# Performance work log

Measured on AMD Instinct MI355X. Metric: run time of the kernel, lower is better.

## Reference

```python
import jax, jax.numpy as jnp
import numpy as np

N, M, D, G, E = 1024, 1024, 1024, 16, 64  # rois, ref rois, feat_dim, groups, emb_dim
DG = D // G  # 64 per-group dim


def _make_boxes(k, n):
    k1, k2 = jax.random.split(k)
    xy = jax.random.uniform(k1, (n, 2), dtype=jnp.float32) * 500.0
    wh = jax.random.uniform(k2, (n, 2), dtype=jnp.float32) * 100.0 + 1.0
    return jnp.concatenate([xy, xy + wh], axis=1)  # [n,4] xmin,ymin,xmax,ymax


def setup_inputs() -> dict:
    key = jax.random.key(0)
    ks = jax.random.split(key, 10)
    s = 0.02
    return {
        "roi_feat": jax.random.normal(ks[0], (N, D), dtype=jnp.float32),
        "ref_feat": jax.random.normal(ks[1], (M, D), dtype=jnp.float32),
        "rois1": _make_boxes(ks[2], N),
        "rois2": _make_boxes(ks[3], M),
        "Wq": jax.random.normal(ks[4], (D, D), dtype=jnp.float32) * s,
        "bq": jnp.zeros((D,), jnp.float32),
        "Wk": jax.random.normal(ks[5], (D, D), dtype=jnp.float32) * s,
        "bk": jnp.zeros((D,), jnp.float32),
        "Wg": jax.random.normal(ks[6], (G, E), dtype=jnp.float32) * s,
        "bg": jnp.zeros((G,), jnp.float32),
        "Wv": jax.random.normal(ks[7], (G, DG, D), dtype=jnp.float32) * s,
        "bv": jnp.zeros((D,), jnp.float32),
    }


def _position_matrix(bbox, ref_bbox):
    # bbox [N,4], ref_bbox [M,4] -> [N,M,4]
    def parts(b):
        xmin, ymin, xmax, ymax = b[:, 0], b[:, 1], b[:, 2], b[:, 3]
        w = xmax - xmin + 1.0
        h = ymax - ymin + 1.0
        cx = 0.5 * (xmin + xmax)
        cy = 0.5 * (ymin + ymax)
        return w, h, cx, cy

    w, h, cx, cy = parts(bbox)            # [N]
    wr, hr, cxr, cyr = parts(ref_bbox)    # [M]
    dx = jnp.log(jnp.abs((cx[:, None] - cxr[None, :]) / w[:, None]) + 1e-3)
    dy = jnp.log(jnp.abs((cy[:, None] - cyr[None, :]) / h[:, None]) + 1e-3)
    dw = jnp.log(w[:, None] / wr[None, :])
    dh = jnp.log(h[:, None] / hr[None, :])
    return jnp.stack([dx, dy, dw, dh], axis=2)  # [N,M,4]


def _position_embedding(pos_mat, feat_dim=64, wave_length=1000.0):
    fr = jnp.arange(feat_dim // 8, dtype=jnp.float32)            # [8]
    dim_mat = jnp.power(wave_length, (8.0 / feat_dim) * fr)      # [8]
    div = pos_mat[..., None] * 100.0 / dim_mat                   # [N,M,4,8]
    emb = jnp.concatenate([jnp.sin(div), jnp.cos(div)], axis=3)  # [N,M,4,16]
    return emb.reshape(pos_mat.shape[0], pos_mat.shape[1], -1)   # [N,M,64]


def reference(roi_feat, ref_feat, rois1, rois2, Wq, bq, Wk, bk, Wg, bg, Wv, bv):
    # position embedding: [N,M,E]
    pos_emb = _position_embedding(_position_matrix(rois1, rois2), feat_dim=E)
    # Wgs 1x1 conv (E -> G) + relu -> aff_weight [N,G,M]
    aff_weight = jax.nn.relu(jnp.einsum("nme,ge->ngm", pos_emb, Wg) + bg[None, :, None])
    # grouped q/k projections
    q = (roi_feat @ Wq + bq).reshape(N, G, DG)   # [N,G,dg]
    k = (ref_feat @ Wk + bk).reshape(M, G, DG)   # [M,G,dg]
    aff = jnp.einsum("ngd,mgd->ngm", q, k) * (1.0 / np.sqrt(DG))
    weighted = jnp.log(aff_weight + 1e-6) + aff  # [N,G,M]
    sm = jax.nn.softmax(weighted, axis=2)
    out_t = jnp.einsum("ngm,md->ngd", sm, ref_feat)          # [N,G,D]
    out = jnp.einsum("ngd,god->ngo", out_t, Wv).reshape(N, D) + bv  # grouped 1x1 conv
    return out
```

## Files before the change

### kernel.cpp

```cpp
#include <hip/hip_runtime.h>
#include <hip/hip_fp16.h>
#include <cstddef>

#define N_ 1024
#define M_ 1024
#define D_ 1024
#define G_ 16
#define DG_ 64

typedef __bf16 bf16x8 __attribute__((ext_vector_type(8)));
typedef _Float16 f16x8 __attribute__((ext_vector_type(8)));
typedef float f32x4 __attribute__((ext_vector_type(4)));

__device__ __forceinline__ size_t qkf_idx(int g, int rb, int ks, int lane) {
    return ((((size_t)(g * 64 + rb)) * 2 + ks) * 64 + lane) * 8;
}
__device__ __forceinline__ size_t vf_idx(int g, int ot, int mc, int lane) {
    return ((((size_t)(g * 4 + ot)) * 32 + mc) * 64 + lane) * 8;
}
__device__ __forceinline__ size_t awt_idx(int g, int mb, int n, int quad) {
    return (((size_t)(mb * 1024 + n)) * 16 + g) * 16 + quad * 4;
}

__global__ __launch_bounds__(256)
void fused_mid2(const float* __restrict__ roi, const float* __restrict__ ref,
                const float* __restrict__ Wq, const float* __restrict__ Wk,
                const float* __restrict__ Wv,
                const float* __restrict__ bq, const float* __restrict__ bk,
                __bf16* __restrict__ Qf, __bf16* __restrict__ Kf,
                __bf16* __restrict__ Vf,
                const float* __restrict__ rois1, const float* __restrict__ rois2,
                const float* __restrict__ Wg, const float* __restrict__ bg,
                __half* __restrict__ AWt)
{
    __shared__ __align__(16) char smem[36864];
    const int b = blockIdx.x;
    const int tid = threadIdx.x;
    const int w = tid >> 6, lane = tid & 63;
    const int quad = lane >> 4, l15 = lane & 15;

    if (b < 192) {
        const int t = b;
        const int z = t >> 6, t6 = t & 63;
        const float* A = (z == 0) ? roi : ref;
        const float* Wf = (z == 0) ? Wq : (z == 1) ? Wk : Wv;
        const int i0 = (t6 >> 3) * 128, j0 = (t6 & 7) * 128;
        const int iw = (w & 1) * 64, jw = (w >> 1) * 64;

        __bf16(*As)[72] = (__bf16(*)[72])smem;
        __bf16(*Bs)[72] = (__bf16(*)[72])(smem + 18432);

        f32x4 acc[4][4] = {};

        for (int k0 = 0; k0 < D_; k0 += 64) {
            __syncthreads();
            #pragma unroll
            for (int it = 0; it < 8; ++it) {
                const int idx = tid + 256 * it;
                const int row = idx >> 4, c = idx & 15;
                float4 a = *(const float4*)&A[(size_t)(i0 + row) * D_ + k0 + c * 4];
                __bf16 p[4] = {(__bf16)a.x, (__bf16)a.y, (__bf16)a.z, (__bf16)a.w};
                *(uint2*)&As[row][c * 4] = *(const uint2*)p;
            }
            if (z < 2) {
                #pragma unroll
                for (int it = 0; it < 8; ++it) {
                    const int idx = tid + 256 * it;
                    const int jl = idx & 127;
                    const int kc = idx >> 7;
                    const float* src = &Wf[(size_t)(k0 + kc * 4) * D_ + j0 + jl];
                    __bf16 p[4];
                    p[0] = (__bf16)src[0];
                    p[1] = (__bf16)src[D_];
                    p[2] = (__bf16)src[2 * D_];
                    p[3] = (__bf16)src[3 * D_];
                    *(uint2*)&Bs[jl][kc * 4] = *(const uint2*)p;
                }
            } else {
                #pragma unroll
                for (int it = 0; it < 8; ++it) {
                    const int idx = tid + 256 * it;
                    const int row = idx >> 4, c = idx & 15;
                    float4 a = *(const float4*)&Wf[(size_t)(j0 + row) * D_ + k0 + c * 4];
                    __bf16 p[4] = {(__bf16)a.x, (__bf16)a.y, (__bf16)a.z, (__bf16)a.w};
                    *(uint2*)&Bs[row][c * 4] = *(const uint2*)p;
                }
            }
            __syncthreads();
            #pragma unroll
            for (int ks = 0; ks < 2; ++ks) {
                bf16x8 af[4], bfr[4];
                #pragma unroll
                for (int t4 = 0; t4 < 4; ++t4) {
                    af[t4]  = *(const bf16x8*)&As[iw + t4 * 16 + l15][ks * 32 + quad * 8];
                    bfr[t4] = *(const bf16x8*)&Bs[jw + t4 * 16 + l15][ks * 32 + quad * 8];
                }
                #pragma unroll
                for (int ti = 0; ti < 4; ++ti)
                    #pragma unroll
                    for (int tj = 0; tj < 4; ++tj)
                        acc[ti][tj] = __builtin_amdgcn_mfma_f32_16x16x32_bf16(
                            af[ti], bfr[tj], acc[ti][tj], 0, 0, 0);
            }
        }

        if (z < 2) {
            const float* bias = (z == 0) ? bq : bk;
            __bf16* dst = (z == 0) ? Qf : Kf;
            const float scale = (z == 0) ? 0.125f : 1.0f;
            #pragma unroll
            for (int ti = 0; ti < 4; ++ti) {
                const int rb = (i0 + iw + ti * 16) >> 4;
                #pragma unroll
                for (int tj = 0; tj < 4; ++tj) {
                    const int go = j0 + jw + tj * 16 + l15;
                    const int g = go >> 6, ks = (go >> 5) & 1;
                    const int lanef = ((go >> 3) & 3) * 16;
                    const int jf = go & 7;
                    const float bb = bias[go];
                    __bf16* base = dst + qkf_idx(g, rb, ks, 0) + jf;
                    #pragma unroll
                    for (int r = 0; r < 4; ++r)
                        base[(size_t)(lanef + quad * 4 + r) * 8] =
                            (__bf16)((acc[ti][tj][r] + bb) * scale);
                }
            }
        } else {
            #pragma unroll
            for (int ti = 0; ti < 4; ++ti) {
                const int mbase = i0 + iw + ti * 16 + quad * 4;
                const int mc = mbase >> 5, quadv = (mbase >> 3) & 3, jb = mbase & 7;
                #pragma unroll
                for (int tj = 0; tj < 4; ++tj) {
                    const int go = j0 + jw + tj * 16 + l15;
                    const int g = go >> 6, ot = (go >> 4) & 3, o15 = go & 15;
                    __bf16 p[4];
                    #pragma unroll
                    for (int r = 0; r < 4; ++r) p[r] = (__bf16)acc[ti][tj][r];
                    *(uint2*)&Vf[vf_idx(g, ot, mc, quadv * 16 + o15) + jb] =
                        *(const uint2*)p;
                }
            }
        }
        return;
    }

    const int n = b - 192;

    const float xmin = rois1[n * 4 + 0], ymin = rois1[n * 4 + 1];
    const float xmax = rois1[n * 4 + 2], ymax = rois1[n * 4 + 3];
    const float wn  = xmax - xmin + 1.f, hn  = ymax - ymin + 1.f;
    const float cxn = 0.5f * (xmin + xmax), cyn = 0.5f * (ymin + ymax);
    const float rwn = 1.0f / wn, rhn = 1.0f / hn;
    const float lwn = __logf(wn), lhn = __logf(hn);

    f16x8 wgf[2];
    #pragma unroll
    for (int ks = 0; ks < 2; ++ks) {
        const float* p = &Wg[l15 * 64 + ks * 32 + quad * 8];
        float4 a = *(const float4*)p;
        float4 bb = *(const float4*)(p + 4);
        wgf[ks][0] = (_Float16)a.x; wgf[ks][1] = (_Float16)a.y;
        wgf[ks][2] = (_Float16)a.z; wgf[ks][3] = (_Float16)a.w;
        wgf[ks][4] = (_Float16)bb.x; wgf[ks][5] = (_Float16)bb.y;
        wgf[ks][6] = (_Float16)bb.z; wgf[ks][7] = (_Float16)bb.w;
    }
    const float bgv = bg[l15];

    const float fr8[8] = {100.0f, 42.16965f, 17.782794f, 7.4989421f,
                          3.1622777f, 1.3335214f, 0.56234133f, 0.23713737f};
    const float phase = (quad & 1) ? 1.5707963267948966f : 0.f;

    for (int mq = 0; mq < 4; ++mq) {
        const int m0w = mq * 256 + w * 64;
        #pragma unroll
        for (int ti = 0; ti < 4; ++ti) {
            const int mt0 = m0w + ti * 16;
            const int m = mt0 + l15;
            float4 r2 = *(const float4*)&rois2[m * 4];
            const float wr  = r2.z - r2.x + 1.f, hr  = r2.w - r2.y + 1.f;
            const float cxr = 0.5f * (r2.x + r2.z), cyr = 0.5f * (r2.y + r2.w);

            const float f0 = __logf(fabsf((cxn - cxr) * rwn) + 0.001f);
            const float f1 = __logf(fabsf((cyn - cyr) * rhn) + 0.001f);
            const float f2 = lwn - __logf(wr);
            const float f3 = lhn - __logf(hr);
            const float fa = (quad & 2) ? f1 : f0;
            const float fb = (quad & 2) ? f3 : f2;

            f32x4 acc = {};
            #pragma unroll
            for (int ks = 0; ks < 2; ++ks) {
                const float feat = ks ? fb : fa;
                f16x8 ef;
                #pragma unroll
                for (int j = 0; j < 8; ++j)
                    ef[j] = (_Float16)__sinf(fmaf(feat, fr8[j], phase));
                acc = __builtin_amdgcn_mfma_f32_16x16x32_f16(ef, wgf[ks], acc, 0, 0, 0);
            }

            __half p[4];
            #pragma unroll
            for (int r = 0; r < 4; ++r)
                p[r] = __float2half(fmaxf(acc[r] + bgv, 0.f) + 1e-6f);
            *(uint2*)&AWt[awt_idx(l15, mt0 >> 4, n, quad)] = *(const uint2*)p;
        }
    }
}

__global__ __launch_bounds__(256)
void attn_mfma(const __bf16* __restrict__ Qf, const __bf16* __restrict__ Kf,
               const __bf16* __restrict__ Vf, const __half* __restrict__ AWt,
               const float* __restrict__ bv, float* __restrict__ out)
{
    __shared__ __align__(16) char smem[17664];

    const int tid = threadIdx.x;
    const int w = tid >> 6, lane = tid & 63;
    const int quad = lane >> 4, l15 = lane & 15;
    const int nb = blockIdx.x, n0 = nb * 16, g = blockIdx.y;

    __bf16(*Psw)[72] = (__bf16(*)[72])(smem + w * 2304);
    float(*accb)[64][17] = (float(*)[64][17])smem;
    float(*lsb)[16] = (float(*)[16])(smem + 17408);

    bf16x8 qf[2];
    qf[0] = *(const bf16x8*)&Qf[qkf_idx(g, nb, 0, lane)];
    qf[1] = *(const bf16x8*)&Qf[qkf_idx(g, nb, 1, lane)];

    f32x4 acc[4] = {};
    float llocal = 0.f;

    #pragma unroll
    for (int t64 = 0; t64 < 4; ++t64) {
        const int mt = w * 4 + t64;

        f32x4 s[4];
        #pragma unroll
        for (int t = 0; t < 4; ++t) {
            bf16x8 ka0 = *(const bf16x8*)&Kf[qkf_idx(g, mt * 4 + t, 0, lane)];
            bf16x8 ka1 = *(const bf16x8*)&Kf[qkf_idx(g, mt * 4 + t, 1, lane)];
            f32x4 z = {};
            __builtin_amdgcn_s_setprio(1);
            z = __builtin_amdgcn_mfma_f32_16x16x32_bf16(ka0, qf[0], z, 0, 0, 0);
            s[t] = __builtin_amdgcn_mfma_f32_16x16x32_bf16(ka1, qf[1], z, 0, 0, 0);
            __builtin_amdgcn_s_setprio(0);
        }

        #pragma unroll
        for (int t = 0; t < 4; ++t) {
            uint2 au = *(const uint2*)&AWt[awt_idx(g, mt * 4 + t, n0 + l15, quad)];
            const __half* a4 = (const __half*)&au;
            __bf16 pk[4];
            #pragma unroll
            for (int r = 0; r < 4; ++r) {
                const float p = __half2float(a4[r]) * __expf(s[t][r]);
                llocal += p;
                pk[r] = (__bf16)p;
            }
            *(uint2*)&Psw[l15][t * 16 + quad * 4] = *(const uint2*)pk;
        }

        #pragma unroll
        for (int mcl = 0; mcl < 2; ++mcl) {
            bf16x8 pbf = *(const bf16x8*)&Psw[l15][mcl * 32 + quad * 8];
            __builtin_amdgcn_s_setprio(1);
            #pragma unroll
            for (int ot = 0; ot < 4; ++ot) {
                bf16x8 va = *(const bf16x8*)&Vf[vf_idx(g, ot, mt * 2 + mcl, lane)];
                acc[ot] = __builtin_amdgcn_mfma_f32_16x16x32_bf16(va, pbf, acc[ot], 0, 0, 0);
            }
            __builtin_amdgcn_s_setprio(0);
        }
    }

    llocal += __shfl_xor(llocal, 16, 64);
    llocal += __shfl_xor(llocal, 32, 64);

    __syncthreads();

    #pragma unroll
    for (int ot = 0; ot < 4; ++ot)
        #pragma unroll
        for (int r = 0; r < 4; ++r)
            accb[w][ot * 16 + quad * 4 + r][l15] = acc[ot][r];
    if (quad == 0) lsb[w][l15] = llocal;
    __syncthreads();

    const float lt = lsb[0][l15] + lsb[1][l15] + lsb[2][l15] + lsb[3][l15];
    const float inv = 1.f / lt;
    #pragma unroll
    for (int r = 0; r < 4; ++r) {
        const int o = w * 16 + quad * 4 + r;
        const int ogl = g * 64 + o;
        const float v = accb[0][o][l15] + accb[1][o][l15] +
                        accb[2][o][l15] + accb[3][o][l15];
        out[(size_t)(n0 + l15) * D_ + ogl] = v * inv + bv[ogl];
    }
}

extern "C" void kernel_launch(void* const* d_in, const int* in_sizes, int n_in,
                              void* d_out, int out_size, void* d_ws, size_t ws_size,
                              hipStream_t stream) {
    const float* roi_feat = (const float*)d_in[0];
    const float* ref_feat = (const float*)d_in[1];
    const float* rois1    = (const float*)d_in[2];
    const float* rois2    = (const float*)d_in[3];
    const float* Wq       = (const float*)d_in[4];
    const float* bq       = (const float*)d_in[5];
    const float* Wk       = (const float*)d_in[6];
    const float* bk       = (const float*)d_in[7];
    const float* Wg       = (const float*)d_in[8];
    const float* bg       = (const float*)d_in[9];
    const float* Wv       = (const float*)d_in[10];
    const float* bv       = (const float*)d_in[11];
    float* out = (float*)d_out;

    char* ws = (char*)d_ws;
    __bf16* Qf  = (__bf16*)(ws + 0);
    __bf16* Kf  = (__bf16*)(ws + (2u << 20));
    __bf16* Vf  = (__bf16*)(ws + (4u << 20));
    __half* AWt = (__half*)(ws + (6u << 20));

    dim3 blk(256);
    fused_mid2<<<dim3(1216), blk, 0, stream>>>(roi_feat, ref_feat, Wq, Wk, Wv,
                                               bq, bk, Qf, Kf, Vf,
                                               rois1, rois2, Wg, bg, AWt);
    attn_mfma<<<dim3(64, 16), blk, 0, stream>>>(Qf, Kf, Vf, AWt, bv, out);
}
```

Before: 137.7 us.

## Halve GEMM tile width and prefetch next K-slice into registers

The projection GEMM section now uses 128x64 output tiles instead of 128x128, doubling its block count from 192 to 384 so more CUs get work. It also adds register prefetching: the global loads for the next K-slice are issued right after the shared-memory stores, so they overlap the MFMA work on the current slice. Shared memory use drops to match the smaller B tile. In exchange, A tiles are re-read twice as often and register pressure rises from the prefetch buffers.

```diff
diff --git a/kernel.cpp b/kernel.cpp
--- a/kernel.cpp
+++ b/kernel.cpp
@@ -23,7 +23,7 @@
 }
 
 __global__ __launch_bounds__(256)
-void fused_mid2(const float* __restrict__ roi, const float* __restrict__ ref,
+void fused_mid3(const float* __restrict__ roi, const float* __restrict__ ref,
                 const float* __restrict__ Wq, const float* __restrict__ Wk,
                 const float* __restrict__ Wv,
                 const float* __restrict__ bq, const float* __restrict__ bk,
@@ -33,72 +33,129 @@
                 const float* __restrict__ Wg, const float* __restrict__ bg,
                 __half* __restrict__ AWt)
 {
-    __shared__ __align__(16) char smem[36864];
+    __shared__ __align__(16) char smem[27648];
     const int b = blockIdx.x;
     const int tid = threadIdx.x;
     const int w = tid >> 6, lane = tid & 63;
     const int quad = lane >> 4, l15 = lane & 15;
 
-    if (b < 192) {
-        const int t = b;
-        const int z = t >> 6, t6 = t & 63;
+    if (b < 384) {
+        const int z = b >> 7, t6 = b & 127;
         const float* A = (z == 0) ? roi : ref;
         const float* Wf = (z == 0) ? Wq : (z == 1) ? Wk : Wv;
-        const int i0 = (t6 >> 3) * 128, j0 = (t6 & 7) * 128;
-        const int iw = (w & 1) * 64, jw = (w >> 1) * 64;
+        const int i0 = (t6 >> 4) * 128, j0 = (t6 & 15) * 64;
+        const int iw = (w & 1) * 64, jw = (w >> 1) * 32;
 
         __bf16(*As)[72] = (__bf16(*)[72])smem;
         __bf16(*Bs)[72] = (__bf16(*)[72])(smem + 18432);
 
-        f32x4 acc[4][4] = {};
-
-        for (int k0 = 0; k0 < D_; k0 += 64) {
-            __syncthreads();
+        f32x4 acc[4][2] = {};
+
+        float4 apf[8];
+        float4 bpf4[4];
+        float  bpfs[16];
+
+        {
             #pragma unroll
             for (int it = 0; it < 8; ++it) {
                 const int idx = tid + 256 * it;
                 const int row = idx >> 4, c = idx & 15;
-                float4 a = *(const float4*)&A[(size_t)(i0 + row) * D_ + k0 + c * 4];
-                __bf16 p[4] = {(__bf16)a.x, (__bf16)a.y, (__bf16)a.z, (__bf16)a.w};
+                apf[it] = *(const float4*)&A[(size_t)(i0 + row) * D_ + c * 4];
+            }
+            if (z < 2) {
+                #pragma unroll
+                for (int it = 0; it < 4; ++it) {
+                    const int idx = tid + 256 * it;
+                    const int jl = idx & 63, kc = idx >> 6;
+                    const float* src = &Wf[(size_t)(kc * 4) * D_ + j0 + jl];
+                    bpfs[it * 4 + 0] = src[0];
+                    bpfs[it * 4 + 1] = src[D_];
+                    bpfs[it * 4 + 2] = src[2 * D_];
+                    bpfs[it * 4 + 3] = src[3 * D_];
+                }
+            } else {
+                #pragma unroll
+                for (int it = 0; it < 4; ++it) {
+                    const int idx = tid + 256 * it;
+                    const int row = idx >> 4, c = idx & 15;
+                    bpf4[it] = *(const float4*)&Wf[(size_t)(j0 + row) * D_ + c * 4];
+                }
+            }
+        }
+
+        for (int k0 = 0; k0 < D_; k0 += 64) {
+            __syncthreads();
+            #pragma unroll
+            for (int it = 0; it < 8; ++it) {
+                const int idx = tid + 256 * it;
+                const int row = idx >> 4, c = idx & 15;
+                __bf16 p[4] = {(__bf16)apf[it].x, (__bf16)apf[it].y,
+                               (__bf16)apf[it].z, (__bf16)apf[it].w};
                 *(uint2*)&As[row][c * 4] = *(const uint2*)p;
             }
             if (z < 2) {
                 #pragma unroll
+                for (int it = 0; it < 4; ++it) {
+                    const int idx = tid + 256 * it;
+                    const int jl = idx & 63, kc = idx >> 6;
+                    __bf16 p[4] = {(__bf16)bpfs[it * 4 + 0], (__bf16)bpfs[it * 4 + 1],
+                                   (__bf16)bpfs[it * 4 + 2], (__bf16)bpfs[it * 4 + 3]};
+                    *(uint2*)&Bs[jl][kc * 4] = *(const uint2*)p;
+                }
+            } else {
+                #pragma unroll
+                for (int it = 0; it < 4; ++it) {
+                    const int idx = tid + 256 * it;
+                    const int row = idx >> 4, c = idx & 15;
+                    __bf16 p[4] = {(__bf16)bpf4[it].x, (__bf16)bpf4[it].y,
+                                   (__bf16)bpf4[it].z, (__bf16)bpf4[it].w};
+                    *(uint2*)&Bs[row][c * 4] = *(const uint2*)p;
+                }
+            }
+            __syncthreads();
+
+            const int kn = k0 + 64;
+            if (kn < D_) {
+                #pragma unroll
                 for (int it = 0; it < 8; ++it) {
                     const int idx = tid + 256 * it;
-                    const int jl = idx & 127;
-                    const int kc = idx >> 7;
-                    const float* src = &Wf[(size_t)(k0 + kc * 4) * D_ + j0 + jl];
-                    __bf16 p[4];
-                    p[0] = (__bf16)src[0];
-                    p[1] = (__bf16)src[D_];
-                    p[2] = (__bf16)src[2 * D_];
-                    p[3] = (__bf16)src[3 * D_];
-                    *(uint2*)&Bs[jl][kc * 4] = *(const uint2*)p;
-                }
-            } else {
-                #pragma unroll
-                for (int it = 0; it < 8; ++it) {
-                    const int idx = tid + 256 * it;
                     const int row = idx >> 4, c = idx & 15;
-                    float4 a = *(const float4*)&Wf[(size_t)(j0 + row) * D_ + k0 + c * 4];
-                    __bf16 p[4] = {(__bf16)a.x, (__bf16)a.y, (__bf16)a.z, (__bf16)a.w};
-                    *(uint2*)&Bs[row][c * 4] = *(const uint2*)p;
-                }
-            }
-            __syncthreads();
+                    apf[it] = *(const float4*)&A[(size_t)(i0 + row) * D_ + kn + c * 4];
+                }
+                if (z < 2) {
+                    #pragma unroll
+                    for (int it = 0; it < 4; ++it) {
+                        const int idx = tid + 256 * it;
+                        const int jl = idx & 63, kc = idx >> 6;
+                        const float* src = &Wf[(size_t)(kn + kc * 4) * D_ + j0 + jl];
+                        bpfs[it * 4 + 0] = src[0];
+                        bpfs[it * 4 + 1] = src[D_];
+                        bpfs[it * 4 + 2] = src[2 * D_];
+                        bpfs[it * 4 + 3] = src[3 * D_];
+                    }
+                } else {
+                    #pragma unroll
+                    for (int it = 0; it < 4; ++it) {
+                        const int idx = tid + 256 * it;
+                        const int row = idx >> 4, c = idx & 15;
+                        bpf4[it] = *(const float4*)&Wf[(size_t)(j0 + row) * D_ + kn + c * 4];
+                    }
+                }
+            }
+
             #pragma unroll
             for (int ks = 0; ks < 2; ++ks) {
-                bf16x8 af[4], bfr[4];
-                #pragma unroll
-                for (int t4 = 0; t4 < 4; ++t4) {
-                    af[t4]  = *(const bf16x8*)&As[iw + t4 * 16 + l15][ks * 32 + quad * 8];
+                bf16x8 af[4], bfr[2];
+                #pragma unroll
+                for (int t4 = 0; t4 < 4; ++t4)
+                    af[t4] = *(const bf16x8*)&As[iw + t4 * 16 + l15][ks * 32 + quad * 8];
+                #pragma unroll
+                for (int t4 = 0; t4 < 2; ++t4)
                     bfr[t4] = *(const bf16x8*)&Bs[jw + t4 * 16 + l15][ks * 32 + quad * 8];
-                }
                 #pragma unroll
                 for (int ti = 0; ti < 4; ++ti)
                     #pragma unroll
-                    for (int tj = 0; tj < 4; ++tj)
+                    for (int tj = 0; tj < 2; ++tj)
                         acc[ti][tj] = __builtin_amdgcn_mfma_f32_16x16x32_bf16(
                             af[ti], bfr[tj], acc[ti][tj], 0, 0, 0);
             }
@@ -112,7 +169,7 @@
             for (int ti = 0; ti < 4; ++ti) {
                 const int rb = (i0 + iw + ti * 16) >> 4;
                 #pragma unroll
-                for (int tj = 0; tj < 4; ++tj) {
+                for (int tj = 0; tj < 2; ++tj) {
                     const int go = j0 + jw + tj * 16 + l15;
                     const int g = go >> 6, ks = (go >> 5) & 1;
                     const int lanef = ((go >> 3) & 3) * 16;
@@ -131,7 +188,7 @@
                 const int mbase = i0 + iw + ti * 16 + quad * 4;
                 const int mc = mbase >> 5, quadv = (mbase >> 3) & 3, jb = mbase & 7;
                 #pragma unroll
-                for (int tj = 0; tj < 4; ++tj) {
+                for (int tj = 0; tj < 2; ++tj) {
                     const int go = j0 + jw + tj * 16 + l15;
                     const int g = go >> 6, ot = (go >> 4) & 3, o15 = go & 15;
                     __bf16 p[4];
@@ -145,7 +202,7 @@
         return;
     }
 
-    const int n = b - 192;
+    const int n = b - 384;
 
     const float xmin = rois1[n * 4 + 0], ymin = rois1[n * 4 + 1];
     const float xmax = rois1[n * 4 + 2], ymax = rois1[n * 4 + 3];
@@ -323,7 +380,7 @@
     __half* AWt = (__half*)(ws + (6u << 20));
 
     dim3 blk(256);
-    fused_mid2<<<dim3(1216), blk, 0, stream>>>(roi_feat, ref_feat, Wq, Wk, Wv,
+    fused_mid3<<<dim3(1408), blk, 0, stream>>>(roi_feat, ref_feat, Wq, Wk, Wv,
                                                bq, bk, Qf, Kf, Vf,
                                                rois1, rois2, Wg, bg, AWt);
     attn_mfma<<<dim3(64, 16), blk, 0, stream>>>(Qf, Kf, Vf, AWt, bv, out);
```

New measurement: 139.7 us. About the same (+1.4%).

## Retile AWt layout per (group, n-block) and prefetch attention operands

Applied to the files above, without the earlier changes.

Changes the AWt position-weight layout so each (group, 16-row n-block, m-block) slab is contiguous, making attention reads of AWt coalesced. The producer kernel writes in the new layout. The attention kernel now loads all K, AWt and V fragments for an iteration up front, with the loop kept rolled and launch bounds set for two blocks per CU, to raise memory-level parallelism. The output store becomes one float4 per lane. The risks are higher register pressure and scattered writes in the producer kernel.

```diff
diff --git a/kernel.cpp b/kernel.cpp
--- a/kernel.cpp
+++ b/kernel.cpp
@@ -18,8 +18,9 @@
 __device__ __forceinline__ size_t vf_idx(int g, int ot, int mc, int lane) {
     return ((((size_t)(g * 4 + ot)) * 32 + mc) * 64 + lane) * 8;
 }
-__device__ __forceinline__ size_t awt_idx(int g, int mb, int n, int quad) {
-    return (((size_t)(mb * 1024 + n)) * 16 + g) * 16 + quad * 4;
+__device__ __forceinline__ size_t awt_idx(int g, int nb, int mb, int n16, int q4) {
+    size_t slab = ((size_t)(g * 64 + nb) * 64 + mb);
+    return slab * 256 + n16 * 16 + q4 * 4;
 }
 
 __global__ __launch_bounds__(256)
@@ -146,6 +147,7 @@
     }
 
     const int n = b - 192;
+    const int nbw = n >> 4, n16 = n & 15;
 
     const float xmin = rois1[n * 4 + 0], ymin = rois1[n * 4 + 1];
     const float xmax = rois1[n * 4 + 2], ymax = rois1[n * 4 + 3];
@@ -203,15 +205,15 @@
             #pragma unroll
             for (int r = 0; r < 4; ++r)
                 p[r] = __float2half(fmaxf(acc[r] + bgv, 0.f) + 1e-6f);
-            *(uint2*)&AWt[awt_idx(l15, mt0 >> 4, n, quad)] = *(const uint2*)p;
-        }
-    }
-}
-
-__global__ __launch_bounds__(256)
-void attn_mfma(const __bf16* __restrict__ Qf, const __bf16* __restrict__ Kf,
-               const __bf16* __restrict__ Vf, const __half* __restrict__ AWt,
-               const float* __restrict__ bv, float* __restrict__ out)
+            *(uint2*)&AWt[awt_idx(l15, nbw, mt0 >> 4, n16, quad)] = *(const uint2*)p;
+        }
+    }
+}
+
+__global__ __launch_bounds__(256, 2)
+void attn_mfma6(const __bf16* __restrict__ Qf, const __bf16* __restrict__ Kf,
+                const __bf16* __restrict__ Vf, const __half* __restrict__ AWt,
+                const float* __restrict__ bv, float* __restrict__ out)
 {
     __shared__ __align__(16) char smem[17664];
 
@@ -231,26 +233,40 @@
     f32x4 acc[4] = {};
     float llocal = 0.f;
 
-    #pragma unroll
+    #pragma unroll 1
     for (int t64 = 0; t64 < 4; ++t64) {
         const int mt = w * 4 + t64;
 
+        bf16x8 ka0[4], ka1[4];
+        uint2 au[4];
+        bf16x8 va[8];
+        #pragma unroll
+        for (int t = 0; t < 4; ++t) {
+            ka0[t] = *(const bf16x8*)&Kf[qkf_idx(g, mt * 4 + t, 0, lane)];
+            ka1[t] = *(const bf16x8*)&Kf[qkf_idx(g, mt * 4 + t, 1, lane)];
+        }
+        #pragma unroll
+        for (int t = 0; t < 4; ++t)
+            au[t] = *(const uint2*)&AWt[awt_idx(g, nb, mt * 4 + t, l15, quad)];
+        #pragma unroll
+        for (int mcl = 0; mcl < 2; ++mcl)
+            #pragma unroll
+            for (int ot = 0; ot < 4; ++ot)
+                va[mcl * 4 + ot] = *(const bf16x8*)&Vf[vf_idx(g, ot, mt * 2 + mcl, lane)];
+
         f32x4 s[4];
         #pragma unroll
         for (int t = 0; t < 4; ++t) {
-            bf16x8 ka0 = *(const bf16x8*)&Kf[qkf_idx(g, mt * 4 + t, 0, lane)];
-            bf16x8 ka1 = *(const bf16x8*)&Kf[qkf_idx(g, mt * 4 + t, 1, lane)];
             f32x4 z = {};
             __builtin_amdgcn_s_setprio(1);
-            z = __builtin_amdgcn_mfma_f32_16x16x32_bf16(ka0, qf[0], z, 0, 0, 0);
-            s[t] = __builtin_amdgcn_mfma_f32_16x16x32_bf16(ka1, qf[1], z, 0, 0, 0);
+            z = __builtin_amdgcn_mfma_f32_16x16x32_bf16(ka0[t], qf[0], z, 0, 0, 0);
+            s[t] = __builtin_amdgcn_mfma_f32_16x16x32_bf16(ka1[t], qf[1], z, 0, 0, 0);
             __builtin_amdgcn_s_setprio(0);
         }
 
         #pragma unroll
         for (int t = 0; t < 4; ++t) {
-            uint2 au = *(const uint2*)&AWt[awt_idx(g, mt * 4 + t, n0 + l15, quad)];
-            const __half* a4 = (const __half*)&au;
+            const __half* a4 = (const __half*)&au[t];
             __bf16 pk[4];
             #pragma unroll
             for (int r = 0; r < 4; ++r) {
@@ -266,10 +282,9 @@
             bf16x8 pbf = *(const bf16x8*)&Psw[l15][mcl * 32 + quad * 8];
             __builtin_amdgcn_s_setprio(1);
             #pragma unroll
-            for (int ot = 0; ot < 4; ++ot) {
-                bf16x8 va = *(const bf16x8*)&Vf[vf_idx(g, ot, mt * 2 + mcl, lane)];
-                acc[ot] = __builtin_amdgcn_mfma_f32_16x16x32_bf16(va, pbf, acc[ot], 0, 0, 0);
-            }
+            for (int ot = 0; ot < 4; ++ot)
+                acc[ot] = __builtin_amdgcn_mfma_f32_16x16x32_bf16(
+                    va[mcl * 4 + ot], pbf, acc[ot], 0, 0, 0);
             __builtin_amdgcn_s_setprio(0);
         }
     }
@@ -289,14 +304,18 @@
 
     const float lt = lsb[0][l15] + lsb[1][l15] + lsb[2][l15] + lsb[3][l15];
     const float inv = 1.f / lt;
+    float4 ov;
+    float* ovp = (float*)&ov;
     #pragma unroll
     for (int r = 0; r < 4; ++r) {
         const int o = w * 16 + quad * 4 + r;
         const int ogl = g * 64 + o;
         const float v = accb[0][o][l15] + accb[1][o][l15] +
                         accb[2][o][l15] + accb[3][o][l15];
-        out[(size_t)(n0 + l15) * D_ + ogl] = v * inv + bv[ogl];
-    }
+        ovp[r] = v * inv + bv[ogl];
+    }
+    const int ogl0 = g * 64 + w * 16 + quad * 4;
+    *(float4*)&out[(size_t)(n0 + l15) * D_ + ogl0] = ov;
 }
 
 extern "C" void kernel_launch(void* const* d_in, const int* in_sizes, int n_in,
@@ -326,5 +345,5 @@
     fused_mid2<<<dim3(1216), blk, 0, stream>>>(roi_feat, ref_feat, Wq, Wk, Wv,
                                                bq, bk, Qf, Kf, Vf,
                                                rois1, rois2, Wg, bg, AWt);
-    attn_mfma<<<dim3(64, 16), blk, 0, stream>>>(Qf, Kf, Vf, AWt, bv, out);
-}
+    attn_mfma6<<<dim3(64, 16), blk, 0, stream>>>(Qf, Kf, Vf, AWt, bv, out);
+}
```

Measured after the change: 147.0 us. 1.07x slower.
